# Kernel tuning notes

Measured on AMD Instinct MI355X. Metric: run time of the kernel, lower is better.

Reference implementation:

```python
import jax, jax.numpy as jnp
import numpy as np

ROT_DELTA = 1  # rotation_delta from __init__
BN_EPS = 1e-3  # keras BatchNormalization default epsilon


def conv_dirac(signal, bc_idx, bc_w, W, b):
    """Template-based intrinsic mesh conv (dirac patch operator).

    signal: [N, D]; bc_idx/bc_w: [N, Rr, A, 3]; W: [T, Rr, A, D]; b: [T].
    Returns [N, K, T] with K = A // ROT_DELTA rotations.
    """
    gathered = signal[bc_idx]  # [N, Rr, A, 3, D] irregular gather
    interp = jnp.einsum('vrai,vraid->vrad', bc_w, gathered)  # barycentric interp
    A = interp.shape[2]
    rots = np.arange(0, A, ROT_DELTA)
    # Rotating the (small) template weights is equivalent to rolling the
    # interpolated signal along the angular axis, but far cheaper.
    W_rot = jnp.stack([jnp.roll(W, int(r), axis=2) for r in rots])  # [K, T, Rr, A, D]
    return jnp.einsum('vrad,ktrad->vkt', interp, W_rot) + b  # [N, K, T]


def angular_max_pool(x):
    # Select, per vertex, the rotation whose response has maximal L2 norm.
    k = jnp.argmax(jnp.linalg.norm(x, axis=-1), axis=1)  # [N]
    return jnp.take_along_axis(x, k[:, None, None], axis=1)[:, 0]  # [N, T]


def batch_norm(x, gamma, beta):
    mu = jnp.mean(x, axis=0, keepdims=True)
    var = jnp.var(x, axis=0, keepdims=True)
    return gamma * (x - mu) * jax.lax.rsqrt(var + BN_EPS) + beta


def setup_inputs() -> dict:
    key = jax.random.key(0)
    ks = jax.random.split(key, 6)
    N, Rr, A, D, T = 80000, 5, 8, 32, 32
    signal = jax.random.normal(ks[0], (N, D), dtype=jnp.float32)
    bc_idx = jax.random.randint(ks[1], (N, Rr, A, 3), 0, N)
    bc_w = jax.random.uniform(ks[2], (N, Rr, A, 3), dtype=jnp.float32)
    bc_w = bc_w / jnp.sum(bc_w, axis=-1, keepdims=True)  # barycentric coords sum to 1
    W1 = jax.random.normal(ks[3], (T, Rr, A, D), dtype=jnp.float32) * 0.05
    W2 = jax.random.normal(ks[4], (T, Rr, A, D), dtype=jnp.float32) * 0.05
    return {
        'signal': signal, 'bc_idx': bc_idx, 'bc_w': bc_w,
        'W1': W1, 'b1': jnp.zeros((T,), jnp.float32),
        'gamma1': jnp.ones((T,), jnp.float32), 'beta1': jnp.zeros((T,), jnp.float32),
        'W2': W2, 'b2': jnp.zeros((T,), jnp.float32),
        'gamma2': jnp.ones((T,), jnp.float32), 'beta2': jnp.zeros((T,), jnp.float32),
    }


def reference(signal, bc_idx, bc_w, W1, b1, gamma1, beta1, W2, b2, gamma2, beta2):
    # Branch 1: conv -> angular max-pool -> BN -> relu
    s = conv_dirac(signal, bc_idx, bc_w, W1, b1)
    s = angular_max_pool(s)
    s = batch_norm(s, gamma1, beta1)
    s = jax.nn.relu(s)
    # Branch 2: conv -> angular max-pool -> BN
    s = conv_dirac(s, bc_idx, bc_w, W2, b2)
    s = angular_max_pool(s)
    s = batch_norm(s, gamma2, beta2)
    # Residual add (input_dim == amt_templates -> no rescale branch) + activation
    return jax.nn.relu(s + signal)
```

## Files before the change

kernel.cpp:

```cpp
#include <hip/hip_runtime.h>
#include <math.h>

#define RR 5
#define AA 8
#define DD 32
#define TT 32
#define KK 8

#define RT2 0.70710678118654752f

typedef float v2f __attribute__((ext_vector_type(2)));
typedef float v4f __attribute__((ext_vector_type(4)));

static __device__ __forceinline__ v2f pkfma(v2f a, v2f b, v2f c) {
#if __has_builtin(__builtin_elementwise_fma)
    return __builtin_elementwise_fma(a, b, c);
#else
    v2f r; r.x = fmaf(a.x, b.x, c.x); r.y = fmaf(a.y, b.y, c.y); return r;
#endif
}
static __device__ __forceinline__ v4f pkfma4(v4f a, v4f b, v4f c) {
#if __has_builtin(__builtin_elementwise_fma)
    return __builtin_elementwise_fma(a, b, c);
#else
    v4f r;
    r.x = fmaf(a.x, b.x, c.x); r.y = fmaf(a.y, b.y, c.y);
    r.z = fmaf(a.z, b.z, c.z); r.w = fmaf(a.w, b.w, c.w);
    return r;
#endif
}

__global__ void prep_kernel(const float* __restrict__ W1, const float* __restrict__ W2,
                            float* __restrict__ Ws1, float* __restrict__ Ws2,
                            double* __restrict__ dz, float* __restrict__ fz) {
    int b = blockIdx.x;
    int tid = threadIdx.x;
    if (b == 0 && tid < 128) { dz[tid] = 0.0; fz[tid] = 0.f; }
    int which = (b >= 20) ? 1 : 0;
    const float* __restrict__ W = which ? W2 : W1;
    float* __restrict__ Ws = which ? Ws2 : Ws1;
    int idx = (b - which * 20) * 256 + tid;
    if (idx >= TT * RR * DD) return;
    int d = idx & 31;
    int tr = idx >> 5;
    int t = tr / 5;
    int r = tr - t * 5;
    float xa[8];
    #pragma unroll
    for (int a = 0; a < 8; ++a) xa[a] = W[(tr * 8 + a) * 32 + d];
    float s0 = xa[0] + xa[4], d0 = xa[0] - xa[4];
    float s1 = xa[1] + xa[5], d1 = xa[1] - xa[5];
    float s2 = xa[2] + xa[6], d2 = xa[2] - xa[6];
    float s3 = xa[3] + xa[7], d3 = xa[3] - xa[7];
    float s02 = s0 + s2, s13 = s1 + s3;
    float F0 = s02 + s13, F4 = s02 - s13;
    float R2 = s0 - s2, I2 = s3 - s1;
    float u = RT2 * (d1 - d3), v = RT2 * (d1 + d3);
    float R1 = d0 + u, R3 = d0 - u;
    float I1 = -d2 - v, I3 = d2 - v;
    float* o = &Ws[(size_t)((r * 32 + d) * 256 + t * 8)];
    o[0] = F0; o[1] = F4; o[2] = R1; o[3] = I1;
    o[4] = R2; o[5] = I2; o[6] = R3; o[7] = I3;
}

__global__ __launch_bounds__(256, 2)
void fused_conv_kernel(const float* __restrict__ sig,
                       const int* __restrict__ bc_idx,
                       const float* __restrict__ bc_w,
                       const float* __restrict__ Wsg,
                       const float* __restrict__ bias,
                       float* __restrict__ s_out,
                       double* __restrict__ sums,
                       double* __restrict__ sumsq,
                       int N) {
    __shared__ float Is[64 * 260];
    __shared__ float StS[256];

    int tid = threadIdx.x;
    int vBase = blockIdx.x * 64;
    int lane = tid & 63;
    int wv = tid >> 6;

    int vg = lane & 7;
    int tg = lane >> 3;
    int v0L = wv * 16 + vg;
    int v1L = v0L + 8;
    int v0 = vBase + v0L;
    int v1 = vBase + v1L;

    int d4 = lane & 7;
    int g8 = lane >> 3;

    v2f A0[2][4], A1[2][4], A2[2][4], A3[2][4];
    #pragma unroll
    for (int vv = 0; vv < 2; ++vv)
        #pragma unroll
        for (int j = 0; j < 4; ++j) {
            A0[vv][j] = (v2f){0.f, 0.f}; A1[vv][j] = (v2f){0.f, 0.f};
            A2[vv][j] = (v2f){0.f, 0.f}; A3[vv][j] = (v2f){0.f, 0.f};
        }

    for (int r = 0; r < RR; ++r) {
        #pragma unroll
        for (int vv0 = 0; vv0 < 2; ++vv0) {
            int vvL = wv * 16 + vv0 * 8 + g8;
            int vgl = vBase + vvL;
            int vgc = (vgl < N) ? vgl : (N - 1);
            int base = vgc * 120 + r * 24;
            int idxv[24]; float wbc[24];
            const int4* ib = (const int4*)(bc_idx + base);
            const float4* fb = (const float4*)(bc_w + base);
            #pragma unroll
            for (int q = 0; q < 6; ++q) {
                *(int4*)&idxv[q * 4] = ib[q];
                *(float4*)&wbc[q * 4] = fb[q];
            }
            v4f xa[8];
            #pragma unroll
            for (int a = 0; a < 8; ++a) {
                int i0 = idxv[a * 3 + 0];
                int i1 = idxv[a * 3 + 1];
                int i2 = idxv[a * 3 + 2];
                v4f r0 = *(const v4f*)&sig[(size_t)i0 * 32 + 4 * d4];
                v4f r1 = *(const v4f*)&sig[(size_t)i1 * 32 + 4 * d4];
                v4f r2 = *(const v4f*)&sig[(size_t)i2 * 32 + 4 * d4];
                float w0 = wbc[a * 3 + 0];
                float w1 = wbc[a * 3 + 1];
                float w2 = wbc[a * 3 + 2];
                v4f w0v = (v4f){w0, w0, w0, w0};
                v4f w1v = (v4f){w1, w1, w1, w1};
                v4f w2v = (v4f){w2, w2, w2, w2};
                xa[a] = pkfma4(w2v, r2, pkfma4(w1v, r1, w0v * r0));
            }
            v4f s0 = xa[0] + xa[4], dd0 = xa[0] - xa[4];
            v4f s1 = xa[1] + xa[5], dd1 = xa[1] - xa[5];
            v4f s2 = xa[2] + xa[6], dd2 = xa[2] - xa[6];
            v4f s3 = xa[3] + xa[7], dd3 = xa[3] - xa[7];
            v4f s02 = s0 + s2, s13 = s1 + s3;
            v4f F0 = s02 + s13, F4 = s02 - s13;
            v4f R2 = s0 - s2, I2 = s3 - s1;
            v4f u = RT2 * (dd1 - dd3), vt_ = RT2 * (dd1 + dd3);
            v4f R1 = dd0 + u, R3 = dd0 - u;
            v4f I1 = -dd2 - vt_, I3 = dd2 - vt_;
            float* ob = &Is[vvL * 260 + d4 * 32 + (d4 >> 2) * 4];
            #pragma unroll
            for (int di = 0; di < 4; ++di) {
                *(v4f*)&ob[di * 8]     = (v4f){F0[di], F4[di], R1[di], I1[di]};
                *(v4f*)&ob[di * 8 + 4] = (v4f){R2[di], I2[di], R3[di], I3[di]};
            }
        }
        asm volatile("s_waitcnt lgkmcnt(0)" ::: "memory");
        __builtin_amdgcn_sched_barrier(0);

        const float* wrb = &Wsg[(size_t)(r * 32) * 256];
        #pragma unroll 2
        for (int dl = 0; dl < 32; ++dl) {
            const float* ip = &Is[v0L * 260 + dl * 8 + (dl >> 4) * 4];
            v4f pa0 = *(const v4f*)&ip[0];
            v4f pb0 = *(const v4f*)&ip[4];
            v4f pa1 = *(const v4f*)&ip[2080];
            v4f pb1 = *(const v4f*)&ip[2084];
            v2f x1_0 = pa0.zw, x1n_0 = {pa0.w, -pa0.z};
            v2f x2_0 = pb0.xy, x2n_0 = {pb0.y, -pb0.x};
            v2f x3_0 = pb0.zw, x3n_0 = {pb0.w, -pb0.z};
            v2f x1_1 = pa1.zw, x1n_1 = {pa1.w, -pa1.z};
            v2f x2_1 = pb1.xy, x2n_1 = {pb1.y, -pb1.x};
            v2f x3_1 = pb1.zw, x3n_1 = {pb1.w, -pb1.z};
            const float* wrow = wrb + dl * 256;
            #pragma unroll
            for (int j = 0; j < 4; ++j) {
                v4f q0 = *(const v4f*)&wrow[(tg + 8 * j) * 8];
                v4f q1 = *(const v4f*)&wrow[(tg + 8 * j) * 8 + 4];
                v2f w2v = {q0.z, q0.z}, w3v = {q0.w, q0.w};
                v2f w4v = {q1.x, q1.x}, w5v = {q1.y, q1.y};
                v2f w6v = {q1.z, q1.z}, w7v = {q1.w, q1.w};
                A0[0][j] = pkfma(pa0.xy, q0.xy, A0[0][j]);
                A1[0][j] = pkfma(x1_0, w2v, A1[0][j]);
                A1[0][j] = pkfma(x1n_0, w3v, A1[0][j]);
                A2[0][j] = pkfma(x2_0, w4v, A2[0][j]);
                A2[0][j] = pkfma(x2n_0, w5v, A2[0][j]);
                A3[0][j] = pkfma(x3_0, w6v, A3[0][j]);
                A3[0][j] = pkfma(x3n_0, w7v, A3[0][j]);
                A0[1][j] = pkfma(pa1.xy, q0.xy, A0[1][j]);
                A1[1][j] = pkfma(x1_1, w2v, A1[1][j]);
                A1[1][j] = pkfma(x1n_1, w3v, A1[1][j]);
                A2[1][j] = pkfma(x2_1, w4v, A2[1][j]);
                A2[1][j] = pkfma(x2n_1, w5v, A2[1][j]);
                A3[1][j] = pkfma(x3_1, w6v, A3[1][j]);
                A3[1][j] = pkfma(x3n_1, w7v, A3[1][j]);
            }
        }
        asm volatile("s_waitcnt lgkmcnt(0)" ::: "memory");
        __builtin_amdgcn_sched_barrier(0);
    }

    float bj[4];
    #pragma unroll
    for (int j = 0; j < 4; ++j) bj[j] = bias[tg + 8 * j];

    float outk[2][8][4];
    #pragma unroll
    for (int vv = 0; vv < 2; ++vv) {
        #pragma unroll
        for (int j = 0; j < 4; ++j) {
            float C0 = A0[vv][j].x, C4 = A0[vv][j].y;
            float R1 = A1[vv][j].x, I1 = A1[vv][j].y;
            float R2 = A2[vv][j].x, I2 = A2[vv][j].y;
            float R3 = A3[vv][j].x, I3 = A3[vv][j].y;
            float e = 0.125f * (C0 + C4), o = 0.125f * (C0 - C4);
            float p = 0.25f * (R1 + R3), q = 0.25f * R2, s = 0.25f * (I1 - I3);
            float a_ = 0.25f * RT2 * (R1 - R3);
            float b_ = 0.25f * RT2 * (I1 + I3);
            float c_ = 0.25f * I2;
            float bb = bj[j];
            outk[vv][0][j] = e + p + q + bb;
            outk[vv][1][j] = o + a_ - b_ - c_ + bb;
            outk[vv][2][j] = e - s - q + bb;
            outk[vv][3][j] = o - a_ - b_ + c_ + bb;
            outk[vv][4][j] = e - p + q + bb;
            outk[vv][5][j] = o - a_ + b_ - c_ + bb;
            outk[vv][6][j] = e + s - q + bb;
            outk[vv][7][j] = o + a_ + b_ + c_ + bb;
        }
    }

    float sel[2][4];
    int vOutA[2]; vOutA[0] = v0; vOutA[1] = v1;
    #pragma unroll
    for (int vv = 0; vv < 2; ++vv) {
        float norms[8];
        #pragma unroll
        for (int k = 0; k < 8; ++k) {
            float nl = 0.f;
            #pragma unroll
            for (int j = 0; j < 4; ++j)
                nl = fmaf(outk[vv][k][j], outk[vv][k][j], nl);
            nl += __shfl_xor(nl, 8);
            nl += __shfl_xor(nl, 16);
            nl += __shfl_xor(nl, 32);
            norms[k] = nl;
        }
        float best = -1.f;
        int bk = 0;
        #pragma unroll
        for (int k = 0; k < 8; ++k) {
            float n = sqrtf(norms[k]);
            if (n > best) { best = n; bk = k; }
        }
        #pragma unroll
        for (int j = 0; j < 4; ++j) sel[vv][j] = 0.f;
        #pragma unroll
        for (int k = 0; k < 8; ++k) {
            if (k == bk) {
                #pragma unroll
                for (int j = 0; j < 4; ++j) sel[vv][j] = outk[vv][k][j];
            }
        }
        if (vOutA[vv] < N) {
            float* o = s_out + (size_t)vOutA[vv] * 32 + tg;
            o[0]  = sel[vv][0];
            o[8]  = sel[vv][1];
            o[16] = sel[vv][2];
            o[24] = sel[vv][3];
        }
    }

    float pa_[4], pb_[4];
    #pragma unroll
    for (int j = 0; j < 4; ++j) {
        float s0 = (v0 < N) ? sel[0][j] : 0.f;
        float s1 = (v1 < N) ? sel[1][j] : 0.f;
        pa_[j] = s0 + s1;
        pb_[j] = fmaf(s0, s0, s1 * s1);
    }
    #pragma unroll
    for (int j = 0; j < 4; ++j) {
        pa_[j] += __shfl_xor(pa_[j], 1);
        pb_[j] += __shfl_xor(pb_[j], 1);
        pa_[j] += __shfl_xor(pa_[j], 2);
        pb_[j] += __shfl_xor(pb_[j], 2);
        pa_[j] += __shfl_xor(pa_[j], 4);
        pb_[j] += __shfl_xor(pb_[j], 4);
    }
    __syncthreads();
    if (vg == 0) {
        #pragma unroll
        for (int j = 0; j < 4; ++j) {
            int t = tg + 8 * j;
            StS[(wv * 32 + t) * 2 + 0] = pa_[j];
            StS[(wv * 32 + t) * 2 + 1] = pb_[j];
        }
    }
    __syncthreads();
    if (tid < 64) {
        int t = tid >> 1, c = tid & 1;
        float s = StS[t * 2 + c] + StS[64 + t * 2 + c] +
                  StS[128 + t * 2 + c] + StS[192 + t * 2 + c];
        if (c == 0) atomicAdd(&sums[t], (double)s);
        else        atomicAdd(&sumsq[t], (double)s);
    }
}

__global__ void finalize_kernel(const double* __restrict__ sums,
                                const double* __restrict__ sumsq,
                                const float* __restrict__ gamma,
                                const float* __restrict__ beta,
                                float* __restrict__ scale,
                                float* __restrict__ shift, int n) {
    int t = threadIdx.x;
    if (t < 32) {
        double mu = sums[t] / (double)n;
        double var = sumsq[t] / (double)n - mu * mu;
        double sc = (double)gamma[t] / sqrt(var + 1e-3);
        scale[t] = (float)sc;
        shift[t] = (float)((double)beta[t] - mu * sc);
    }
}

__global__ void affine_relu_kernel(const float* __restrict__ s,
                                   const float* __restrict__ scale,
                                   const float* __restrict__ shift,
                                   float* __restrict__ o, int n4) {
    int e = blockIdx.x * blockDim.x + threadIdx.x;
    if (e >= n4) return;
    int t0 = (e & 7) * 4;
    float4 x = ((const float4*)s)[e];
    float4 y;
    y.x = fmaxf(fmaf(scale[t0 + 0], x.x, shift[t0 + 0]), 0.f);
    y.y = fmaxf(fmaf(scale[t0 + 1], x.y, shift[t0 + 1]), 0.f);
    y.z = fmaxf(fmaf(scale[t0 + 2], x.z, shift[t0 + 2]), 0.f);
    y.w = fmaxf(fmaf(scale[t0 + 3], x.w, shift[t0 + 3]), 0.f);
    ((float4*)o)[e] = y;
}

__global__ void final_kernel(const float* __restrict__ s,
                             const float* __restrict__ scale,
                             const float* __restrict__ shift,
                             const float* __restrict__ sig,
                             float* __restrict__ o, int n4) {
    int e = blockIdx.x * blockDim.x + threadIdx.x;
    if (e >= n4) return;
    int t0 = (e & 7) * 4;
    float4 x = ((const float4*)s)[e];
    float4 z = ((const float4*)sig)[e];
    float4 y;
    y.x = fmaxf(fmaf(scale[t0 + 0], x.x, shift[t0 + 0]) + z.x, 0.f);
    y.y = fmaxf(fmaf(scale[t0 + 1], x.y, shift[t0 + 1]) + z.y, 0.f);
    y.z = fmaxf(fmaf(scale[t0 + 2], x.z, shift[t0 + 2]) + z.z, 0.f);
    y.w = fmaxf(fmaf(scale[t0 + 3], x.w, shift[t0 + 3]) + z.w, 0.f);
    ((float4*)o)[e] = y;
}

extern "C" void kernel_launch(void* const* d_in, const int* in_sizes, int n_in,
                              void* d_out, int out_size, void* d_ws, size_t ws_size,
                              hipStream_t stream) {
    const float* signal = (const float*)d_in[0];
    const int* bc_idx   = (const int*)d_in[1];
    const float* bc_w   = (const float*)d_in[2];
    const float* W1     = (const float*)d_in[3];
    const float* b1     = (const float*)d_in[4];
    const float* g1     = (const float*)d_in[5];
    const float* be1    = (const float*)d_in[6];
    const float* W2     = (const float*)d_in[7];
    const float* b2     = (const float*)d_in[8];
    const float* g2     = (const float*)d_in[9];
    const float* be2    = (const float*)d_in[10];
    float* out = (float*)d_out;

    const int N = in_sizes[0] / 32;

    char* ws = (char*)d_ws;
    double* sums1  = (double*)ws;
    double* sumsq1 = sums1 + 32;
    double* sums2  = sums1 + 64;
    double* sumsq2 = sums1 + 96;
    float* scale1 = (float*)(ws + 1024);
    float* shift1 = scale1 + 32;
    float* scale2 = scale1 + 64;
    float* shift2 = scale1 + 96;
    float* Ws1 = (float*)(ws + 4096);
    float* Ws2 = Ws1 + RR * DD * TT * 8;
    float* s1  = Ws2 + RR * DD * TT * 8;
    float* sg2 = s1 + (size_t)N * 32;
    float* s2  = sg2 + (size_t)N * 32;

    int nBlocks = (N + 63) / 64;

    prep_kernel<<<40, 256, 0, stream>>>(W1, W2, Ws1, Ws2, (double*)ws, (float*)(ws + 1024));

    fused_conv_kernel<<<nBlocks, 256, 0, stream>>>(signal, bc_idx, bc_w, Ws1, b1, s1,
                                                   sums1, sumsq1, N);
    finalize_kernel<<<1, 32, 0, stream>>>(sums1, sumsq1, g1, be1, scale1, shift1, N);
    affine_relu_kernel<<<(N * 8 + 255) / 256, 256, 0, stream>>>(s1, scale1, shift1, sg2, N * 8);

    fused_conv_kernel<<<nBlocks, 256, 0, stream>>>(sg2, bc_idx, bc_w, Ws2, b2, s2,
                                                   sums2, sumsq2, N);
    finalize_kernel<<<1, 32, 0, stream>>>(sums2, sumsq2, g2, be2, scale2, shift2, N);

    final_kernel<<<(N * 8 + 255) / 256, 256, 0, stream>>>(s2, scale2, shift2, signal, out, N * 8);
}
```

Baseline: 678.4 us.

## Halve LDS staging buffer by splitting FFT-bin contraction into two passes

Shrinks the per-block shared staging buffer from 64x260 to 64x132 floats by storing only four of the eight FFT bins at a time. The other four are held in registers and written to LDS after the first contraction pass, followed by a second pass. The gather loop is also split into two halves to cut live index and weight registers. Launch bounds go from 2 to 3 blocks per CU to raise occupancy. The cost is an extra LDS round trip, extra waits, and more register pressure from the stashed bins.

```diff
diff --git a/kernel.cpp b/kernel.cpp
--- a/kernel.cpp
+++ b/kernel.cpp
@@ -63,7 +63,7 @@
     o[4] = R2; o[5] = I2; o[6] = R3; o[7] = I3;
 }
 
-__global__ __launch_bounds__(256, 2)
+__global__ __launch_bounds__(256, 3)
 void fused_conv_kernel(const float* __restrict__ sig,
                        const int* __restrict__ bc_idx,
                        const float* __restrict__ bc_w,
@@ -73,7 +73,7 @@
                        double* __restrict__ sums,
                        double* __restrict__ sumsq,
                        int N) {
-    __shared__ float Is[64 * 260];
+    __shared__ float Is[64 * 132];
     __shared__ float StS[256];
 
     int tid = threadIdx.x;
@@ -101,36 +101,41 @@
         }
 
     for (int r = 0; r < RR; ++r) {
+        v4f st[2][4];
+
         #pragma unroll
         for (int vv0 = 0; vv0 < 2; ++vv0) {
             int vvL = wv * 16 + vv0 * 8 + g8;
             int vgl = vBase + vvL;
             int vgc = (vgl < N) ? vgl : (N - 1);
             int base = vgc * 120 + r * 24;
-            int idxv[24]; float wbc[24];
             const int4* ib = (const int4*)(bc_idx + base);
             const float4* fb = (const float4*)(bc_w + base);
-            #pragma unroll
-            for (int q = 0; q < 6; ++q) {
-                *(int4*)&idxv[q * 4] = ib[q];
-                *(float4*)&wbc[q * 4] = fb[q];
-            }
             v4f xa[8];
             #pragma unroll
-            for (int a = 0; a < 8; ++a) {
-                int i0 = idxv[a * 3 + 0];
-                int i1 = idxv[a * 3 + 1];
-                int i2 = idxv[a * 3 + 2];
-                v4f r0 = *(const v4f*)&sig[(size_t)i0 * 32 + 4 * d4];
-                v4f r1 = *(const v4f*)&sig[(size_t)i1 * 32 + 4 * d4];
-                v4f r2 = *(const v4f*)&sig[(size_t)i2 * 32 + 4 * d4];
-                float w0 = wbc[a * 3 + 0];
-                float w1 = wbc[a * 3 + 1];
-                float w2 = wbc[a * 3 + 2];
-                v4f w0v = (v4f){w0, w0, w0, w0};
-                v4f w1v = (v4f){w1, w1, w1, w1};
-                v4f w2v = (v4f){w2, w2, w2, w2};
-                xa[a] = pkfma4(w2v, r2, pkfma4(w1v, r1, w0v * r0));
+            for (int hc = 0; hc < 2; ++hc) {
+                int idxv[12]; float wbc[12];
+                #pragma unroll
+                for (int q = 0; q < 3; ++q) {
+                    *(int4*)&idxv[q * 4] = ib[hc * 3 + q];
+                    *(float4*)&wbc[q * 4] = fb[hc * 3 + q];
+                }
+                #pragma unroll
+                for (int a = 0; a < 4; ++a) {
+                    int i0 = idxv[a * 3 + 0];
+                    int i1 = idxv[a * 3 + 1];
+                    int i2 = idxv[a * 3 + 2];
+                    v4f r0 = *(const v4f*)&sig[(size_t)i0 * 32 + 4 * d4];
+                    v4f r1 = *(const v4f*)&sig[(size_t)i1 * 32 + 4 * d4];
+                    v4f r2 = *(const v4f*)&sig[(size_t)i2 * 32 + 4 * d4];
+                    float w0 = wbc[a * 3 + 0];
+                    float w1 = wbc[a * 3 + 1];
+                    float w2 = wbc[a * 3 + 2];
+                    v4f w0v = (v4f){w0, w0, w0, w0};
+                    v4f w1v = (v4f){w1, w1, w1, w1};
+                    v4f w2v = (v4f){w2, w2, w2, w2};
+                    xa[hc * 4 + a] = pkfma4(w2v, r2, pkfma4(w1v, r1, w0v * r0));
+                }
             }
             v4f s0 = xa[0] + xa[4], dd0 = xa[0] - xa[4];
             v4f s1 = xa[1] + xa[5], dd1 = xa[1] - xa[5];
@@ -142,11 +147,11 @@
             v4f u = RT2 * (dd1 - dd3), vt_ = RT2 * (dd1 + dd3);
             v4f R1 = dd0 + u, R3 = dd0 - u;
             v4f I1 = -dd2 - vt_, I3 = dd2 - vt_;
-            float* ob = &Is[vvL * 260 + d4 * 32 + (d4 >> 2) * 4];
+            float* ob = &Is[vvL * 132 + d4 * 16];
             #pragma unroll
             for (int di = 0; di < 4; ++di) {
-                *(v4f*)&ob[di * 8]     = (v4f){F0[di], F4[di], R1[di], I1[di]};
-                *(v4f*)&ob[di * 8 + 4] = (v4f){R2[di], I2[di], R3[di], I3[di]};
+                *(v4f*)&ob[di * 4] = (v4f){F0[di], F4[di], R1[di], I1[di]};
+                st[vv0][di] = (v4f){R2[di], I2[di], R3[di], I3[di]};
             }
         }
         asm volatile("s_waitcnt lgkmcnt(0)" ::: "memory");
@@ -155,35 +160,57 @@
         const float* wrb = &Wsg[(size_t)(r * 32) * 256];
         #pragma unroll 2
         for (int dl = 0; dl < 32; ++dl) {
-            const float* ip = &Is[v0L * 260 + dl * 8 + (dl >> 4) * 4];
+            const float* ip = &Is[v0L * 132 + dl * 4];
             v4f pa0 = *(const v4f*)&ip[0];
-            v4f pb0 = *(const v4f*)&ip[4];
-            v4f pa1 = *(const v4f*)&ip[2080];
-            v4f pb1 = *(const v4f*)&ip[2084];
+            v4f pa1 = *(const v4f*)&ip[1056];
             v2f x1_0 = pa0.zw, x1n_0 = {pa0.w, -pa0.z};
+            v2f x1_1 = pa1.zw, x1n_1 = {pa1.w, -pa1.z};
+            const float* wrow = wrb + dl * 256;
+            #pragma unroll
+            for (int j = 0; j < 4; ++j) {
+                v4f q0 = *(const v4f*)&wrow[(tg + 8 * j) * 8];
+                v2f w2v = {q0.z, q0.z}, w3v = {q0.w, q0.w};
+                A0[0][j] = pkfma(pa0.xy, q0.xy, A0[0][j]);
+                A1[0][j] = pkfma(x1_0, w2v, A1[0][j]);
+                A1[0][j] = pkfma(x1n_0, w3v, A1[0][j]);
+                A0[1][j] = pkfma(pa1.xy, q0.xy, A0[1][j]);
+                A1[1][j] = pkfma(x1_1, w2v, A1[1][j]);
+                A1[1][j] = pkfma(x1n_1, w3v, A1[1][j]);
+            }
+        }
+        asm volatile("s_waitcnt lgkmcnt(0)" ::: "memory");
+        __builtin_amdgcn_sched_barrier(0);
+
+        #pragma unroll
+        for (int vv0 = 0; vv0 < 2; ++vv0) {
+            int vvL = wv * 16 + vv0 * 8 + g8;
+            float* ob = &Is[vvL * 132 + d4 * 16];
+            #pragma unroll
+            for (int di = 0; di < 4; ++di)
+                *(v4f*)&ob[di * 4] = st[vv0][di];
+        }
+        asm volatile("s_waitcnt lgkmcnt(0)" ::: "memory");
+        __builtin_amdgcn_sched_barrier(0);
+
+        #pragma unroll 2
+        for (int dl = 0; dl < 32; ++dl) {
+            const float* ip = &Is[v0L * 132 + dl * 4];
+            v4f pb0 = *(const v4f*)&ip[0];
+            v4f pb1 = *(const v4f*)&ip[1056];
             v2f x2_0 = pb0.xy, x2n_0 = {pb0.y, -pb0.x};
             v2f x3_0 = pb0.zw, x3n_0 = {pb0.w, -pb0.z};
-            v2f x1_1 = pa1.zw, x1n_1 = {pa1.w, -pa1.z};
             v2f x2_1 = pb1.xy, x2n_1 = {pb1.y, -pb1.x};
             v2f x3_1 = pb1.zw, x3n_1 = {pb1.w, -pb1.z};
             const float* wrow = wrb + dl * 256;
             #pragma unroll
             for (int j = 0; j < 4; ++j) {
-                v4f q0 = *(const v4f*)&wrow[(tg + 8 * j) * 8];
                 v4f q1 = *(const v4f*)&wrow[(tg + 8 * j) * 8 + 4];
-                v2f w2v = {q0.z, q0.z}, w3v = {q0.w, q0.w};
                 v2f w4v = {q1.x, q1.x}, w5v = {q1.y, q1.y};
                 v2f w6v = {q1.z, q1.z}, w7v = {q1.w, q1.w};
-                A0[0][j] = pkfma(pa0.xy, q0.xy, A0[0][j]);
-                A1[0][j] = pkfma(x1_0, w2v, A1[0][j]);
-                A1[0][j] = pkfma(x1n_0, w3v, A1[0][j]);
                 A2[0][j] = pkfma(x2_0, w4v, A2[0][j]);
                 A2[0][j] = pkfma(x2n_0, w5v, A2[0][j]);
                 A3[0][j] = pkfma(x3_0, w6v, A3[0][j]);
                 A3[0][j] = pkfma(x3n_0, w7v, A3[0][j]);
-                A0[1][j] = pkfma(pa1.xy, q0.xy, A0[1][j]);
-                A1[1][j] = pkfma(x1_1, w2v, A1[1][j]);
-                A1[1][j] = pkfma(x1n_1, w3v, A1[1][j]);
                 A2[1][j] = pkfma(x2_1, w4v, A2[1][j]);
                 A2[1][j] = pkfma(x2n_1, w5v, A2[1][j]);
                 A3[1][j] = pkfma(x3_1, w6v, A3[1][j]);
```

After: 1.163 ms. 71.5% more time.
